# Performance work log

Hardware: AMD Instinct MI355X
Metric: run time of the kernel (lower is better)

Reference implementation:

```python
import jax, jax.numpy as jnp
import numpy as np

# HRR ops (holoformer): bind = circular convolution via FFT; unbind = circular
# correlation (bind with the approximate inverse), i.e. conj in freq domain.

def _fft(a):
    return jnp.fft.fft(a, axis=-1)

def _bind_f(Fa, Fb):
    return jnp.fft.ifft(Fa * Fb, axis=-1).real

def _unbind_f(Fs, Fk):
    return jnp.fft.ifft(Fs * jnp.conj(Fk), axis=-1).real


def setup_inputs() -> dict:
    key = jax.random.key(0)
    B, S, D = 4, 4096, 1024
    ks = jax.random.split(key, 5)
    scale = 1.0 / np.sqrt(D)
    inp = {
        "x": jax.random.normal(ks[0], (B, S, D), dtype=jnp.float32),
        "Wq": jax.random.normal(ks[1], (D, D), dtype=jnp.float32) * scale,
        "bq": jnp.zeros((D,), jnp.float32),
        "Wk": jax.random.normal(ks[2], (D, D), dtype=jnp.float32) * scale,
        "bk": jnp.zeros((D,), jnp.float32),
        "Wv": jax.random.normal(ks[3], (D, D), dtype=jnp.float32) * scale,
        "bv": jnp.zeros((D,), jnp.float32),
        "Wr": jax.random.normal(ks[4], (D, D), dtype=jnp.float32) * scale,
        "br": jnp.zeros((D,), jnp.float32),
    }
    return inp


def reference(x, Wq, bq, Wk, bk, Wv, bv, Wr, br):
    # tanh-gated linear projections (nn.Linear stores weight as [out, in])
    query = jnp.tanh(jnp.einsum('bsd,ed->bse', x, Wq) + bq)
    keys = jnp.tanh(jnp.einsum('bsd,ed->bse', x, Wk) + bk)
    values = jnp.tanh(jnp.einsum('bsd,ed->bse', x, Wv) + bv)
    remove_query = jnp.tanh(jnp.einsum('bsd,ed->bse', x, Wr) + br)

    # bind(keys, values) and sum over sequence -> s: (B, 1, D)
    x_k = _bind_f(_fft(keys), _fft(values))
    s = x_k.sum(axis=1, keepdims=True)
    Fs = _fft(s)

    # retrieve with query, add
    retrieved = _unbind_f(Fs, _fft(query))
    out = x + retrieved

    # remove: bind(remove_query, unbind(s, remove_query))
    Fr = _fft(remove_query)
    remove_values = _unbind_f(Fs, Fr)
    removes = _bind_f(Fr, _fft(remove_values))
    out = out - removes
    return out
```

## Files before the change

### kernel.cpp

```cpp
#include <hip/hip_runtime.h>
#include <hip/hip_fp16.h>

#define D 1024
#define LOG2D 10
#define S_LEN 4096
#define BATCH 4
#define NROWS (BATCH * S_LEN)
#define PI_F 3.14159265358979323846f

#define SLOT(p) ((p) + ((p) >> 4))
#define FBUF 1088
#define NTW 341

typedef _Float16 f16x8 __attribute__((ext_vector_type(8)));
typedef float f32x4 __attribute__((ext_vector_type(4)));

__device__ __forceinline__ float2 cmul(float2 a, float2 b) {
    return make_float2(a.x * b.x - a.y * b.y, a.x * b.y + a.y * b.x);
}

__device__ __forceinline__ float fast_tanh(float v) {
    float e = __expf(2.0f * v);
    return 1.0f - 2.0f * __builtin_amdgcn_rcpf(e + 1.0f);
}

__device__ __forceinline__ void g2lds16(const void* g, void* l) {
    __builtin_amdgcn_global_load_lds(
        (const __attribute__((address_space(1))) unsigned int*)g,
        (__attribute__((address_space(3))) unsigned int*)l, 16, 0, 0);
}

__global__ __launch_bounds__(256) void convert_all(
    const float* __restrict__ x,
    const float* __restrict__ w0, const float* __restrict__ w1,
    const float* __restrict__ w2, const float* __restrict__ w3,
    __half* __restrict__ xh,
    __half* __restrict__ h0, __half* __restrict__ h1,
    __half* __restrict__ h2, __half* __restrict__ h3)
{
    const int b = blockIdx.x;
    const float* s;
    __half* d;
    int li;
    if (b < 16384) { s = x; d = xh; li = b; }
    else {
        int t = b - 16384;
        int r = t >> 10;
        li = t & 1023;
        s = (r == 0) ? w0 : (r == 1) ? w1 : (r == 2) ? w2 : w3;
        d = (r == 0) ? h0 : (r == 1) ? h1 : (r == 2) ? h2 : h3;
    }
    const int idx = li * 256 + threadIdx.x;
    float4 v = ((const float4*)s)[idx];
    __half2 lo = __floats2half2_rn(v.x, v.y);
    __half2 hi = __floats2half2_rn(v.z, v.w);
    ((__half2*)d)[2 * idx + 0] = lo;
    ((__half2*)d)[2 * idx + 1] = hi;
}

__global__ __launch_bounds__(256, 2) void gemm_mfma2(
    const __half* __restrict__ Xh,
    const __half* __restrict__ W0, const float* __restrict__ b0, __half* __restrict__ O0,
    const __half* __restrict__ W1, const float* __restrict__ b1, __half* __restrict__ O1)
{
    const int idx = blockIdx.x;
    const int xcd = idx & 7;
    const int j = idx >> 3;
    const int n0 = (j & 7) * 128;
    const int m0 = (xcd * 16 + (j >> 3)) * 128;

    __shared__ __align__(16) __half As[128 * 64];
    __shared__ __align__(16) __half B0s[128 * 64];
    __shared__ __align__(16) __half B1s[128 * 64];

    const int tid = threadIdx.x;
    const int wave = tid >> 6;
    const int lane = tid & 63;

    const int srow = lane >> 3;
    const int schunk = (lane & 7) ^ (lane >> 3);

    const __half* gA[4];
    const __half* gB0[4];
    const __half* gB1[4];
    int loff[4];
#pragma unroll
    for (int c = 0; c < 4; ++c) {
        const int rbase = wave * 32 + c * 8;
        gA[c]  = Xh + (size_t)(m0 + rbase + srow) * 1024 + schunk * 8;
        gB0[c] = W0 + (size_t)(n0 + rbase + srow) * 1024 + schunk * 8;
        gB1[c] = W1 + (size_t)(n0 + rbase + srow) * 1024 + schunk * 8;
        loff[c] = rbase * 64;
    }

    const int wm = (wave & 1) * 64;
    const int wn = (wave >> 1) * 64;
    const int quad = lane >> 4;
    const int l15 = lane & 15;

    int aoff[2][4], boff[2][4];
#pragma unroll
    for (int kk = 0; kk < 2; ++kk)
#pragma unroll
        for (int i = 0; i < 4; ++i) {
            const int Ra = wm + i * 16 + l15;
            aoff[kk][i] = Ra * 64 + ((((kk << 2) | quad)) ^ (l15 & 7)) * 8;
            const int Rb = wn + i * 16 + l15;
            boff[kk][i] = Rb * 64 + ((((kk << 2) | quad)) ^ (l15 & 7)) * 8;
        }

    f32x4 acc0[4][4], acc1[4][4];
#pragma unroll
    for (int i = 0; i < 4; ++i)
#pragma unroll
        for (int jj = 0; jj < 4; ++jj) {
            acc0[i][jj] = (f32x4){0.f, 0.f, 0.f, 0.f};
            acc1[i][jj] = (f32x4){0.f, 0.f, 0.f, 0.f};
        }

    for (int kt = 0; kt < 16; ++kt) {
        const int kh = kt * 64;
        __syncthreads();
#pragma unroll
        for (int c = 0; c < 4; ++c) {
            g2lds16(gA[c] + kh,  As  + loff[c]);
            g2lds16(gB0[c] + kh, B0s + loff[c]);
            g2lds16(gB1[c] + kh, B1s + loff[c]);
        }
        __syncthreads();

#pragma unroll
        for (int kk = 0; kk < 2; ++kk) {
            f16x8 af[4], bf0[4], bf1[4];
#pragma unroll
            for (int i = 0; i < 4; ++i) af[i] = *(const f16x8*)(As + aoff[kk][i]);
#pragma unroll
            for (int jj = 0; jj < 4; ++jj) {
                bf0[jj] = *(const f16x8*)(B0s + boff[kk][jj]);
                bf1[jj] = *(const f16x8*)(B1s + boff[kk][jj]);
            }
#pragma unroll
            for (int i = 0; i < 4; ++i)
#pragma unroll
                for (int jj = 0; jj < 4; ++jj) {
                    acc0[i][jj] = __builtin_amdgcn_mfma_f32_16x16x32_f16(af[i], bf0[jj], acc0[i][jj], 0, 0, 0);
                    acc1[i][jj] = __builtin_amdgcn_mfma_f32_16x16x32_f16(af[i], bf1[jj], acc1[i][jj], 0, 0, 0);
                }
        }
    }

#pragma unroll
    for (int jj = 0; jj < 4; ++jj) {
        const int n = n0 + wn + jj * 16 + l15;
        const float bv0 = b0[n];
        const float bv1 = b1[n];
#pragma unroll
        for (int i = 0; i < 4; ++i) {
            const int mbase = m0 + wm + i * 16 + quad * 4;
#pragma unroll
            for (int r = 0; r < 4; ++r) {
                O0[(size_t)(mbase + r) * 1024 + n] = __float2half(fast_tanh(acc0[i][jj][r] + bv0));
                O1[(size_t)(mbase + r) * 1024 + n] = __float2half(fast_tanh(acc1[i][jj][r] + bv1));
            }
        }
    }
}

__device__ __forceinline__ void build_twiddles_r4(float2* Wts, int tid) {
    for (int j = tid; j < NTW; j += 256) {
        int k, m;
        if (j == 0)      { k = 0;      m = 1;   }
        else if (j < 5)  { k = j - 1;  m = 4;   }
        else if (j < 21) { k = j - 5;  m = 16;  }
        else if (j < 85) { k = j - 21; m = 64;  }
        else             { k = j - 85; m = 256; }
        float ang = PI_F * (float)k / (2.0f * (float)m);
        Wts[j] = make_float2(cosf(ang), -sinf(ang));
    }
}

__device__ void fft1024_r4(float2* bufA, float2* bufB, const float2* Wts,
                           float dir, int tid) {
    float2* src = bufA;
    float2* dst = bufB;
    int m = 1;
#pragma unroll
    for (int s = 0; s < 5; ++s) {
        __syncthreads();
        const int k = tid & (m - 1);
        const int jb = tid >> (2 * s);
        float2 x0 = src[SLOT(tid)];
        float2 x1 = src[SLOT(tid + 256)];
        float2 x2 = src[SLOT(tid + 512)];
        float2 x3 = src[SLOT(tid + 768)];
        float2 y1, y2, y3;
        if (s == 0) { y1 = x1; y2 = x2; y3 = x3; }
        else {
            const int soff = (m - 1) / 3;
            float2 t1 = Wts[soff + k];
            t1.y *= dir;
            float2 t2 = cmul(t1, t1);
            float2 t3 = cmul(t1, t2);
            y1 = cmul(x1, t1);
            y2 = cmul(x2, t2);
            y3 = cmul(x3, t3);
        }
        float2 a = make_float2(x0.x + y2.x, x0.y + y2.y);
        float2 b = make_float2(x0.x - y2.x, x0.y - y2.y);
        float2 c = make_float2(y1.x + y3.x, y1.y + y3.y);
        float2 d = make_float2(y1.x - y3.x, y1.y - y3.y);
        float2 e = make_float2(dir * d.y, -dir * d.x);
        const int o = (jb << (2 * s + 2)) + k;
        dst[SLOT(o)]         = make_float2(a.x + c.x, a.y + c.y);
        dst[SLOT(o + m)]     = make_float2(b.x + e.x, b.y + e.y);
        dst[SLOT(o + 2 * m)] = make_float2(a.x - c.x, a.y - c.y);
        dst[SLOT(o + 3 * m)] = make_float2(b.x - e.x, b.y - e.y);
        float2* t = src; src = dst; dst = t;
        m <<= 2;
    }
    __syncthreads();
}

#define ROWS_PER_BLOCK 8
__global__ __launch_bounds__(256) void bind_accum_kernel(
    const __half* __restrict__ K, const __half* __restrict__ V, float2* __restrict__ Fs)
{
    __shared__ __align__(16) float2 bufA[FBUF];
    __shared__ __align__(16) float2 bufB[FBUF];
    __shared__ __align__(16) float2 Wts[NTW];
    const int tid = threadIdx.x;
    build_twiddles_r4(Wts, tid);

    const int row0 = blockIdx.x * ROWS_PER_BLOCK;
    const int b = row0 >> 12;

    float2 accr[4];
#pragma unroll
    for (int h = 0; h < 4; ++h) accr[h] = make_float2(0.f, 0.f);

    for (int r = 0; r < ROWS_PER_BLOCK; ++r) {
        const size_t base = (size_t)(row0 + r) * D;
#pragma unroll
        for (int h = 0; h < 4; ++h) {
            const int j = tid + (h << 8);
            bufA[SLOT(j)] = make_float2(__half2float(K[base + j]), __half2float(V[base + j]));
        }
        fft1024_r4(bufA, bufB, Wts, 1.0f, tid);
#pragma unroll
        for (int h = 0; h < 4; ++h) {
            const int j = tid + (h << 8);
            const int j2 = (D - j) & (D - 1);
            float2 Zt = bufB[SLOT(j)];
            float2 Zc = bufB[SLOT(j2)]; Zc.y = -Zc.y;
            float2 Fk = make_float2(0.5f * (Zt.x + Zc.x), 0.5f * (Zt.y + Zc.y));
            float2 Fv = make_float2(0.5f * (Zt.y - Zc.y), -0.5f * (Zt.x - Zc.x));
            float2 P = cmul(Fk, Fv);
            accr[h].x += P.x; accr[h].y += P.y;
        }
    }
#pragma unroll
    for (int h = 0; h < 4; ++h) {
        const int j = tid + (h << 8);
        atomicAdd(&Fs[(size_t)b * D + j].x, accr[h].x);
        atomicAdd(&Fs[(size_t)b * D + j].y, accr[h].y);
    }
}

__global__ __launch_bounds__(256) void retrieve_kernel(
    const __half* __restrict__ Q, const __half* __restrict__ R,
    const float2* __restrict__ Fs, const float* __restrict__ x, float* __restrict__ out)
{
    __shared__ __align__(16) float2 bufA[FBUF];
    __shared__ __align__(16) float2 bufB[FBUF];
    __shared__ __align__(16) float2 Wts[NTW];
    const int tid = threadIdx.x;
    build_twiddles_r4(Wts, tid);

    const int row = blockIdx.x;
    const int b = row >> 12;
    const size_t base = (size_t)row * D;

#pragma unroll
    for (int h = 0; h < 4; ++h) {
        const int j = tid + (h << 8);
        bufA[SLOT(j)] = make_float2(__half2float(Q[base + j]), __half2float(R[base + j]));
    }
    fft1024_r4(bufA, bufB, Wts, 1.0f, tid);

#pragma unroll
    for (int h = 0; h < 4; ++h) {
        const int j = tid + (h << 8);
        const int j2 = (D - j) & (D - 1);
        float2 Zt = bufB[SLOT(j)];
        float2 Zc = bufB[SLOT(j2)]; Zc.y = -Zc.y;
        float2 Fq = make_float2(0.5f * (Zt.x + Zc.x), 0.5f * (Zt.y + Zc.y));
        float2 Fr = make_float2(0.5f * (Zt.y - Zc.y), -0.5f * (Zt.x - Zc.x));
        float2 g  = make_float2(Fq.x - (Fr.x * Fr.x + Fr.y * Fr.y), -Fq.y);
        float2 Ff = Fs[(size_t)b * D + j];
        bufA[SLOT(j)] = cmul(Ff, g);
    }
    fft1024_r4(bufA, bufB, Wts, -1.0f, tid);

    const float inv = 1.0f / (float)D;
#pragma unroll
    for (int h = 0; h < 4; ++h) {
        const int j = tid + (h << 8);
        out[base + j] = x[base + j] + bufB[SLOT(j)].x * inv;
    }
}

extern "C" void kernel_launch(void* const* d_in, const int* in_sizes, int n_in,
                              void* d_out, int out_size, void* d_ws, size_t ws_size,
                              hipStream_t stream) {
    const float* x  = (const float*)d_in[0];
    const float* Wq = (const float*)d_in[1];
    const float* bq = (const float*)d_in[2];
    const float* Wk = (const float*)d_in[3];
    const float* bk = (const float*)d_in[4];
    const float* Wv = (const float*)d_in[5];
    const float* bv = (const float*)d_in[6];
    const float* Wr = (const float*)d_in[7];
    const float* br = (const float*)d_in[8];
    float* out = (float*)d_out;

    __half* P0 = (__half*)d_ws;
    __half* P1 = (__half*)((char*)d_ws + (size_t)NROWS * D * 2);
    float2* Fs = (float2*)((char*)d_ws + (size_t)NROWS * D * 4);

    __half* Xh  = (__half*)d_out;
    __half* Whk = (__half*)d_out + (size_t)16 * 1024 * 1024;
    __half* Whv = Whk + (size_t)1024 * 1024;
    __half* Whq = Whv + (size_t)1024 * 1024;
    __half* Whr = Whq + (size_t)1024 * 1024;

    convert_all<<<16384 + 4 * 1024, 256, 0, stream>>>(
        x, Wk, Wv, Wq, Wr, Xh, Whk, Whv, Whq, Whr);

    hipMemsetAsync(Fs, 0, (size_t)BATCH * D * sizeof(float2), stream);

    gemm_mfma2<<<1024, 256, 0, stream>>>(Xh, Whk, bk, P0, Whv, bv, P1);
    bind_accum_kernel<<<NROWS / ROWS_PER_BLOCK, 256, 0, stream>>>(P0, P1, Fs);
    gemm_mfma2<<<1024, 256, 0, stream>>>(Xh, Whq, bq, P0, Whr, br, P1);
    retrieve_kernel<<<NROWS, 256, 0, stream>>>(P0, P1, Fs, x, out);
}
```

Measured before the change: 471.8 us.

## Rewrite retrieve FFT as register-resident 32x32 four-step FFT per warp

The retrieve kernel switches from a shared-memory radix-4 FFT with a per-block twiddle table to a 32x32 four-step FFT. Each 32-thread group runs 32-point FFTs in registers and uses one padded LDS transpose per pass. Each 128-thread block now handles four rows instead of one row per 256-thread block. This removes the twiddle-table construction and most LDS round trips and barriers. In exchange it adds high register pressure (two 32-element complex arrays) and twiddles computed on the fly with sincos and recurrence, which may lower occupancy and accuracy. Global loads and stores now use a stride-32 pattern within each row.

```diff
diff --git a/kernel.cpp b/kernel.cpp
--- a/kernel.cpp
+++ b/kernel.cpp
@@ -266,46 +266,127 @@
     }
 }
 
-__global__ __launch_bounds__(256) void retrieve_kernel(
+
+__device__ constexpr int br5(int i) {
+    return ((i & 1) << 4) | ((i & 2) << 2) | (i & 4) | ((i & 8) >> 2) | ((i & 16) >> 4);
+}
+
+template<int INV>
+__device__ __forceinline__ float2 w32c(int k) {
+    constexpr float C[16] = {
+        1.0f, 0.98078528f, 0.92387953f, 0.83146961f,
+        0.70710678f, 0.55557023f, 0.38268343f, 0.19509032f,
+        0.0f, -0.19509032f, -0.38268343f, -0.55557023f,
+        -0.70710678f, -0.83146961f, -0.92387953f, -0.98078528f};
+    constexpr float Sn[16] = {
+        0.0f, 0.19509032f, 0.38268343f, 0.55557023f,
+        0.70710678f, 0.83146961f, 0.92387953f, 0.98078528f,
+        1.0f, 0.98078528f, 0.92387953f, 0.83146961f,
+        0.70710678f, 0.55557023f, 0.38268343f, 0.19509032f};
+    return make_float2(C[k], INV ? Sn[k] : -Sn[k]);
+}
+
+template<int INV>
+__device__ __forceinline__ void fft32(float2* z) {
+#pragma unroll
+    for (int s = 0; s < 5; ++s) {
+#pragma unroll
+        for (int j = 0; j < 16; ++j) {
+            const int half = 1 << s;
+            const int blk = j >> s;
+            const int off = j & (half - 1);
+            const int i0 = (blk << (s + 1)) + off;
+            const int i1 = i0 + half;
+            const float2 w = w32c<INV>(off << (4 - s));
+            const float2 v = cmul(z[i1], w);
+            z[i1] = make_float2(z[i0].x - v.x, z[i0].y - v.y);
+            z[i0] = make_float2(z[i0].x + v.x, z[i0].y + v.y);
+        }
+    }
+}
+
+#define RETR_ROWS 4
+__global__ __launch_bounds__(128) void retrieve_kernel(
     const __half* __restrict__ Q, const __half* __restrict__ R,
     const float2* __restrict__ Fs, const float* __restrict__ x, float* __restrict__ out)
 {
-    __shared__ __align__(16) float2 bufA[FBUF];
-    __shared__ __align__(16) float2 bufB[FBUF];
-    __shared__ __align__(16) float2 Wts[NTW];
+    __shared__ __align__(16) float2 T[RETR_ROWS][33 * 32];
     const int tid = threadIdx.x;
-    build_twiddles_r4(Wts, tid);
-
-    const int row = blockIdx.x;
+    const int lr = tid >> 5;
+    const int t  = tid & 31;
+    const int row = blockIdx.x * RETR_ROWS + lr;
     const int b = row >> 12;
-    const size_t base = (size_t)row * D;
-
-#pragma unroll
-    for (int h = 0; h < 4; ++h) {
-        const int j = tid + (h << 8);
-        bufA[SLOT(j)] = make_float2(__half2float(Q[base + j]), __half2float(R[base + j]));
-    }
-    fft1024_r4(bufA, bufB, Wts, 1.0f, tid);
-
-#pragma unroll
-    for (int h = 0; h < 4; ++h) {
-        const int j = tid + (h << 8);
-        const int j2 = (D - j) & (D - 1);
-        float2 Zt = bufB[SLOT(j)];
-        float2 Zc = bufB[SLOT(j2)]; Zc.y = -Zc.y;
-        float2 Fq = make_float2(0.5f * (Zt.x + Zc.x), 0.5f * (Zt.y + Zc.y));
-        float2 Fr = make_float2(0.5f * (Zt.y - Zc.y), -0.5f * (Zt.x - Zc.x));
-        float2 g  = make_float2(Fq.x - (Fr.x * Fr.x + Fr.y * Fr.y), -Fq.y);
-        float2 Ff = Fs[(size_t)b * D + j];
-        bufA[SLOT(j)] = cmul(Ff, g);
-    }
-    fft1024_r4(bufA, bufB, Wts, -1.0f, tid);
-
-    const float inv = 1.0f / (float)D;
-#pragma unroll
-    for (int h = 0; h < 4; ++h) {
-        const int j = tid + (h << 8);
-        out[base + j] = x[base + j] + bufB[SLOT(j)].x * inv;
+    const size_t base = (size_t)row << 10;
+    float2* Tr = T[lr];
+
+    float2 z[32];
+#pragma unroll
+    for (int n1 = 0; n1 < 32; ++n1) {
+        const int g = (n1 << 5) + t;
+        z[br5(n1)] = make_float2(__half2float(Q[base + g]),
+                                 __half2float(R[base + g]));
+    }
+    fft32<0>(z);
+
+    float sn_, cs_;
+    __sincosf((PI_F / 512.0f) * (float)t, &sn_, &cs_);
+    {
+        const float2 w1 = make_float2(cs_, -sn_);
+        float2 tw = make_float2(1.0f, 0.0f);
+#pragma unroll
+        for (int k1 = 0; k1 < 32; ++k1) { z[k1] = cmul(z[k1], tw); tw = cmul(tw, w1); }
+    }
+
+#pragma unroll
+    for (int k1 = 0; k1 < 32; ++k1) Tr[33 * k1 + t] = z[k1];
+    __syncthreads();
+#pragma unroll
+    for (int n2 = 0; n2 < 32; ++n2) z[br5(n2)] = Tr[33 * t + n2];
+    fft32<0>(z);
+    __syncthreads();
+
+#pragma unroll
+    for (int k2 = 0; k2 < 32; ++k2) Tr[33 * k2 + t] = z[k2];
+    __syncthreads();
+
+    float2 h[32];
+    const float2* FsB = Fs + ((size_t)b << 10);
+    const int mc = (32 - t) & 31;
+    const int me = (t == 0) ? 1 : 0;
+#pragma unroll
+    for (int k2 = 0; k2 < 32; ++k2) {
+        const int ma = (31 - k2 + me) & 31;
+        float2 Zc = Tr[33 * ma + mc];
+        Zc.y = -Zc.y;
+        const float2 Zt = z[k2];
+        const float2 Fq = make_float2(0.5f * (Zt.x + Zc.x), 0.5f * (Zt.y + Zc.y));
+        const float2 Fr = make_float2(0.5f * (Zt.y - Zc.y), -0.5f * (Zt.x - Zc.x));
+        const float2 g2 = make_float2(Fq.x - (Fr.x * Fr.x + Fr.y * Fr.y), -Fq.y);
+        const float2 Ff = FsB[(k2 << 5) + t];
+        h[br5(k2)] = cmul(Ff, g2);
+    }
+
+    fft32<1>(h);
+    {
+        const float2 w1c = make_float2(cs_, sn_);
+        float2 tw = make_float2(1.0f, 0.0f);
+#pragma unroll
+        for (int n1 = 0; n1 < 32; ++n1) { h[n1] = cmul(h[n1], tw); tw = cmul(tw, w1c); }
+    }
+    __syncthreads();
+#pragma unroll
+    for (int n1 = 0; n1 < 32; ++n1) Tr[33 * n1 + t] = h[n1];
+    __syncthreads();
+#pragma unroll
+    for (int k2 = 0; k2 < 32; ++k2) h[br5(k2)] = Tr[33 * t + k2];
+    fft32<1>(h);
+
+    const float* xr = x + base;
+    float* outr = out + base;
+#pragma unroll
+    for (int n2 = 0; n2 < 32; ++n2) {
+        const int g = (n2 << 5) + t;
+        outr[g] = xr[g] + h[n2].x * (1.0f / 1024.0f);
     }
 }
 
@@ -341,5 +422,5 @@
     gemm_mfma2<<<1024, 256, 0, stream>>>(Xh, Whk, bk, P0, Whv, bv, P1);
     bind_accum_kernel<<<NROWS / ROWS_PER_BLOCK, 256, 0, stream>>>(P0, P1, Fs);
     gemm_mfma2<<<1024, 256, 0, stream>>>(Xh, Whq, bq, P0, Whr, br, P1);
-    retrieve_kernel<<<NROWS, 256, 0, stream>>>(P0, P1, Fs, x, out);
-}
+    retrieve_kernel<<<NROWS / RETR_ROWS, 128, 0, stream>>>(P0, P1, Fs, x, out);
+}
```

New measurement: 419.9 us. 1.12x faster.
